# Optimization experiments

Hardware: AMD Instinct MI355X
Metric: run time of the kernel (lower is better)

Reference implementation:

```python
import jax, jax.numpy as jnp
import numpy as np

TEMP = 0.07


def setup_inputs() -> dict:
    key = jax.random.key(0)
    k1, k2 = jax.random.split(key)
    B, m, d = 256, 128, 768
    v_final = jax.random.normal(k1, (B, d), dtype=jnp.float32)
    T_fused = jax.random.normal(k2, (B, m, d), dtype=jnp.float32)
    return {"v_final": v_final, "T_fused": T_fused}


def reference(v_final, T_fused):
    B = v_final.shape[0]
    # [B, B, m] token-level similarities, scaled by temperature
    sim = jnp.einsum('id,jmd->ijm', v_final, T_fused) / TEMP
    # max over text tokens (ColBERT max-sim) -> [B, B]
    sim_max = sim.max(axis=-1)
    targets = jnp.arange(B)
    # symmetric cross-entropy with diagonal targets
    logp_i2t = jax.nn.log_softmax(sim_max, axis=-1)
    logp_t2i = jax.nn.log_softmax(sim_max.T, axis=-1)
    loss_i2t = -jnp.mean(logp_i2t[targets, targets])
    loss_t2i = -jnp.mean(logp_t2i[targets, targets])
    return (loss_i2t + loss_t2i) / 2
```

## Files before the change

kernel.cpp:

```cpp
#include <hip/hip_runtime.h>
#include <hip/hip_bf16.h>

constexpr int BATCH = 256;
constexpr int MTOK  = 128;
constexpr int DDIM  = 768;
constexpr int NV    = BATCH * DDIM;
constexpr float INV_TEMP = 1.0f / 0.07f;

typedef __bf16 bf16;
typedef __bf16 bf16x8 __attribute__((ext_vector_type(8)));
typedef float  f32x4  __attribute__((ext_vector_type(4)));

__global__ __launch_bounds__(256) void pack_v_kernel(
        const float* __restrict__ V, bf16x8* __restrict__ Vq) {
    int c = blockIdx.x * 256 + threadIdx.x;
    int lane = c & 63, fs = c >> 6;
    int ks = fs % 24, g = fs / 24;
    int l15 = lane & 15, quad = lane >> 4;
    const float* src = V + (size_t)(g * 16 + l15) * DDIM + ks * 32 + quad * 8;
    float4 f0 = *(const float4*)(src);
    float4 f1 = *(const float4*)(src + 4);
    bf16x8 o;
    o[0] = (bf16)f0.x; o[1] = (bf16)f0.y; o[2] = (bf16)f0.z; o[3] = (bf16)f0.w;
    o[4] = (bf16)f1.x; o[5] = (bf16)f1.y; o[6] = (bf16)f1.z; o[7] = (bf16)f1.w;
    Vq[c] = o;
}

__global__ __launch_bounds__(256, 2) void gemm_max_kernel(
        const bf16*  __restrict__ Vq,
        const float* __restrict__ T,
        float* __restrict__ Sp) {
    __shared__ char  ldsB[2 * 8192];
    __shared__ float smax[256];

    const int jt   = blockIdx.x >> 1;
    const int nh   = blockIdx.x & 1;
    const int tid  = threadIdx.x;
    const int w    = tid >> 6;
    const int lane = tid & 63;
    const int quad = lane >> 4;
    const int l15  = lane & 15;

    const bf16* aBase[4];
#pragma unroll
    for (int t = 0; t < 4; ++t)
        aBase[t] = Vq + ((size_t)(w * 4 + t) * 24) * 512 + lane * 8;

    const float* gB[2];
    int bwoff[2];
#pragma unroll
    for (int q = 0; q < 2; ++q) {
        int c = q * 256 + tid;
        int row = c >> 3, kp = c & 7;
        gB[q] = T + (size_t)(jt * MTOK + nh * 64 + row) * DDIM + kp * 8;
        bwoff[q] = (kp >> 2) * 4096 + row * 64 + ((kp & 3) << 4);
    }

    int boff[2][4];
#pragma unroll
    for (int h = 0; h < 2; ++h)
#pragma unroll
        for (int tc = 0; tc < 4; ++tc)
            boff[h][tc] = h * 4096 + (tc * 16 + l15) * 64 + quad * 16;

    f32x4 acc[4][4] = {};

    auto cvt_store = [&](float4 a, float4 b, int q, int bufo) {
        bf16x8 o;
        o[0] = (bf16)a.x; o[1] = (bf16)a.y; o[2] = (bf16)a.z; o[3] = (bf16)a.w;
        o[4] = (bf16)b.x; o[5] = (bf16)b.y; o[6] = (bf16)b.z; o[7] = (bf16)b.w;
        *(bf16x8*)(ldsB + bufo + bwoff[q]) = o;
    };

    float4 breg[2][2];
#pragma unroll
    for (int q = 0; q < 2; ++q) {
        float4 r0 = *(const float4*)(gB[q]);
        float4 r1 = *(const float4*)(gB[q] + 4);
        cvt_store(r0, r1, q, 0);
        breg[q][0] = *(const float4*)(gB[q] + 64);
        breg[q][1] = *(const float4*)(gB[q] + 64 + 4);
    }
    bf16x8 apre[2][4];
#pragma unroll
    for (int h = 0; h < 2; ++h)
#pragma unroll
        for (int t = 0; t < 4; ++t)
            apre[h][t] = *(const bf16x8*)(aBase[t] + (size_t)h * 512);
    __syncthreads();

    for (int kk = 0; kk < 12; ++kk) {
        const int buf  = (kk & 1) * 8192;
        const int nbuf = buf ^ 8192;
        if (kk < 11) {
#pragma unroll
            for (int q = 0; q < 2; ++q)
                cvt_store(breg[q][0], breg[q][1], q, nbuf);
        }
        if (kk < 10) {
#pragma unroll
            for (int q = 0; q < 2; ++q) {
                const float* p = gB[q] + (kk + 2) * 64;
                breg[q][0] = *(const float4*)(p);
                breg[q][1] = *(const float4*)(p + 4);
            }
        }
#pragma unroll
        for (int h = 0; h < 2; ++h) {
            const int hs = kk * 2 + h;
            bf16x8 af[4], bb[4];
#pragma unroll
            for (int t = 0; t < 4; ++t) af[t] = apre[h][t];
            if (hs + 2 < 24) {
#pragma unroll
                for (int t = 0; t < 4; ++t)
                    apre[h][t] = *(const bf16x8*)(aBase[t] + (size_t)(hs + 2) * 512);
            }
#pragma unroll
            for (int tc = 0; tc < 4; ++tc)
                bb[tc] = *(const bf16x8*)(ldsB + buf + boff[h][tc]);
#pragma unroll
            for (int tr = 0; tr < 4; ++tr)
#pragma unroll
                for (int tc = 0; tc < 4; ++tc)
                    acc[tr][tc] = __builtin_amdgcn_mfma_f32_16x16x32_bf16(
                        af[tr], bb[tc], acc[tr][tc], 0, 0, 0);
        }
        __syncthreads();
    }

#pragma unroll
    for (int tr = 0; tr < 4; ++tr) {
#pragma unroll
        for (int r = 0; r < 4; ++r) {
            float v = fmaxf(fmaxf(acc[tr][0][r], acc[tr][1][r]),
                            fmaxf(acc[tr][2][r], acc[tr][3][r]));
            v = fmaxf(v, __shfl_xor(v, 1, 64));
            v = fmaxf(v, __shfl_xor(v, 2, 64));
            v = fmaxf(v, __shfl_xor(v, 4, 64));
            v = fmaxf(v, __shfl_xor(v, 8, 64));
            if (l15 == 0)
                smax[w * 64 + tr * 16 + quad * 4 + r] = v;
        }
    }
    __syncthreads();
    Sp[((size_t)nh * BATCH + jt) * BATCH + tid] = smax[tid] * INV_TEMP;
}

__global__ __launch_bounds__(64) void ce1_kernel(
        const float* __restrict__ Sp, float* __restrict__ partial) {
    const int t = blockIdx.x;
    const int l = threadIdx.x;
    const float* Sp0 = Sp;
    const float* Sp1 = Sp + BATCH * BATCH;

    float vr[4], vc[4];
#pragma unroll
    for (int p = 0; p < 4; ++p) {
        int j = p * 64 + l;
        vr[p] = fmaxf(Sp0[j * BATCH + t], Sp1[j * BATCH + t]);
        int i = p * 64 + l;
        vc[p] = fmaxf(Sp0[t * BATCH + i], Sp1[t * BATCH + i]);
    }
    float mr = fmaxf(fmaxf(vr[0], vr[1]), fmaxf(vr[2], vr[3]));
    float mc = fmaxf(fmaxf(vc[0], vc[1]), fmaxf(vc[2], vc[3]));
    for (int o = 32; o > 0; o >>= 1) {
        mr = fmaxf(mr, __shfl_xor(mr, o, 64));
        mc = fmaxf(mc, __shfl_xor(mc, o, 64));
    }
    float sr = 0.f, sc = 0.f;
#pragma unroll
    for (int p = 0; p < 4; ++p) {
        sr += expf(vr[p] - mr);
        sc += expf(vc[p] - mc);
    }
    for (int o = 32; o > 0; o >>= 1) {
        sr += __shfl_xor(sr, o, 64);
        sc += __shfl_xor(sc, o, 64);
    }
    if (l == 0) {
        float diag = fmaxf(Sp0[t * BATCH + t], Sp1[t * BATCH + t]);
        partial[t] = 0.5f * ((mr + logf(sr)) + (mc + logf(sc))) - diag;
    }
}

__global__ __launch_bounds__(256) void ce2_kernel(
        const float* __restrict__ partial, float* __restrict__ out) {
    const int i = threadIdx.x;
    float term = partial[i];
    for (int o = 32; o > 0; o >>= 1) term += __shfl_down(term, o, 64);
    __shared__ float ps[4];
    if ((i & 63) == 0) ps[i >> 6] = term;
    __syncthreads();
    if (i == 0) out[0] = (ps[0] + ps[1] + ps[2] + ps[3]) / (float)BATCH;
}

extern "C" void kernel_launch(void* const* d_in, const int* in_sizes, int n_in,
                              void* d_out, int out_size, void* d_ws, size_t ws_size,
                              hipStream_t stream) {
    const float* v = (const float*)d_in[0];
    const float* T = (const float*)d_in[1];

    bf16*  Vq = (bf16*)d_ws;
    float* Sp = (float*)((char*)d_ws + (size_t)NV * sizeof(bf16));
    float* partial = Sp + 2 * BATCH * BATCH;

    pack_v_kernel<<<96, 256, 0, stream>>>(v, (bf16x8*)Vq);
    gemm_max_kernel<<<512, 256, 0, stream>>>(Vq, T, Sp);
    ce1_kernel<<<256, 64, 0, stream>>>(Sp, partial);
    ce2_kernel<<<1, 256, 0, stream>>>(partial, (float*)d_out);
}
```

Baseline: 163.5 us.

## Deepen GEMM LDS pipeline to four slabs and fuse CE reduction via atomics

The GEMM kernel's B-tile staging moves from a double buffer to a four-slab LDS ring. Two k-slabs are prefetched into registers and converted per iteration, which halves the number of __syncthreads and puts more global loads in flight. Separately, the final loss reduction kernel is removed: the out scalar is zeroed in the pack kernel and each CE block atomically adds its scaled term, saving one launch. The extra LDS and registers may cut occupancy, and the atomic float sum makes the result order-dependent.

```diff
diff --git a/kernel.cpp b/kernel.cpp
--- a/kernel.cpp
+++ b/kernel.cpp
@@ -12,7 +12,9 @@
 typedef float  f32x4  __attribute__((ext_vector_type(4)));
 
 __global__ __launch_bounds__(256) void pack_v_kernel(
-        const float* __restrict__ V, bf16x8* __restrict__ Vq) {
+        const float* __restrict__ V, bf16x8* __restrict__ Vq,
+        float* __restrict__ out) {
+    if (blockIdx.x == 0 && threadIdx.x == 0) out[0] = 0.f;
     int c = blockIdx.x * 256 + threadIdx.x;
     int lane = c & 63, fs = c >> 6;
     int ks = fs % 24, g = fs / 24;
@@ -30,7 +32,7 @@
         const bf16*  __restrict__ Vq,
         const float* __restrict__ T,
         float* __restrict__ Sp) {
-    __shared__ char  ldsB[2 * 8192];
+    __shared__ char  ldsB[4 * 8192];
     __shared__ float smax[256];
 
     const int jt   = blockIdx.x >> 1;
@@ -56,31 +58,33 @@
         bwoff[q] = (kp >> 2) * 4096 + row * 64 + ((kp & 3) << 4);
     }
 
-    int boff[2][4];
-#pragma unroll
-    for (int h = 0; h < 2; ++h)
-#pragma unroll
-        for (int tc = 0; tc < 4; ++tc)
-            boff[h][tc] = h * 4096 + (tc * 16 + l15) * 64 + quad * 16;
+    int boff[4];
+#pragma unroll
+    for (int tc = 0; tc < 4; ++tc)
+        boff[tc] = (tc * 16 + l15) * 64 + quad * 16;
 
     f32x4 acc[4][4] = {};
 
-    auto cvt_store = [&](float4 a, float4 b, int q, int bufo) {
+    auto cvt_store = [&](const float4* r, int q, int bufo) {
         bf16x8 o;
-        o[0] = (bf16)a.x; o[1] = (bf16)a.y; o[2] = (bf16)a.z; o[3] = (bf16)a.w;
-        o[4] = (bf16)b.x; o[5] = (bf16)b.y; o[6] = (bf16)b.z; o[7] = (bf16)b.w;
+        o[0] = (bf16)r[0].x; o[1] = (bf16)r[0].y; o[2] = (bf16)r[0].z; o[3] = (bf16)r[0].w;
+        o[4] = (bf16)r[1].x; o[5] = (bf16)r[1].y; o[6] = (bf16)r[1].z; o[7] = (bf16)r[1].w;
         *(bf16x8*)(ldsB + bufo + bwoff[q]) = o;
     };
 
-    float4 breg[2][2];
-#pragma unroll
-    for (int q = 0; q < 2; ++q) {
-        float4 r0 = *(const float4*)(gB[q]);
-        float4 r1 = *(const float4*)(gB[q] + 4);
-        cvt_store(r0, r1, q, 0);
-        breg[q][0] = *(const float4*)(gB[q] + 64);
-        breg[q][1] = *(const float4*)(gB[q] + 64 + 4);
-    }
+    float4 breg[2][2][2];
+
+#pragma unroll
+    for (int sp = 0; sp < 2; ++sp)
+#pragma unroll
+        for (int q = 0; q < 2; ++q) {
+            float4 r[2];
+            r[0] = *(const float4*)(gB[q] + sp * 64);
+            r[1] = *(const float4*)(gB[q] + sp * 64 + 4);
+            cvt_store(r, q, sp * 8192);
+            breg[sp][q][0] = *(const float4*)(gB[q] + (sp + 2) * 64);
+            breg[sp][q][1] = *(const float4*)(gB[q] + (sp + 2) * 64 + 4);
+        }
     bf16x8 apre[2][4];
 #pragma unroll
     for (int h = 0; h < 2; ++h)
@@ -89,36 +93,40 @@
             apre[h][t] = *(const bf16x8*)(aBase[t] + (size_t)h * 512);
     __syncthreads();
 
-    for (int kk = 0; kk < 12; ++kk) {
-        const int buf  = (kk & 1) * 8192;
-        const int nbuf = buf ^ 8192;
-        if (kk < 11) {
-#pragma unroll
-            for (int q = 0; q < 2; ++q)
-                cvt_store(breg[q][0], breg[q][1], q, nbuf);
-        }
-        if (kk < 10) {
-#pragma unroll
-            for (int q = 0; q < 2; ++q) {
-                const float* p = gB[q] + (kk + 2) * 64;
-                breg[q][0] = *(const float4*)(p);
-                breg[q][1] = *(const float4*)(p + 4);
+    for (int p = 0; p < 6; ++p) {
+        if (p < 5) {
+#pragma unroll
+            for (int sp = 0; sp < 2; ++sp)
+#pragma unroll
+                for (int q = 0; q < 2; ++q)
+                    cvt_store(breg[sp][q], q, ((2 * p + 2 + sp) & 3) * 8192);
+        }
+        if (p < 4) {
+#pragma unroll
+            for (int sp = 0; sp < 2; ++sp)
+#pragma unroll
+                for (int q = 0; q < 2; ++q) {
+                    const float* ptr = gB[q] + (2 * p + 4 + sp) * 64;
+                    breg[sp][q][0] = *(const float4*)(ptr);
+                    breg[sp][q][1] = *(const float4*)(ptr + 4);
+                }
+        }
+#pragma unroll
+        for (int hh = 0; hh < 4; ++hh) {
+            const int hs   = p * 4 + hh;
+            const int slab = hs >> 1;
+            const int bbase = (slab & 3) * 8192 + (hs & 1) * 4096;
+            bf16x8 af[4], bb[4];
+#pragma unroll
+            for (int t = 0; t < 4; ++t) af[t] = apre[hh & 1][t];
+            if (hs + 2 < 24) {
+#pragma unroll
+                for (int t = 0; t < 4; ++t)
+                    apre[hh & 1][t] = *(const bf16x8*)(aBase[t] + (size_t)(hs + 2) * 512);
             }
-        }
-#pragma unroll
-        for (int h = 0; h < 2; ++h) {
-            const int hs = kk * 2 + h;
-            bf16x8 af[4], bb[4];
-#pragma unroll
-            for (int t = 0; t < 4; ++t) af[t] = apre[h][t];
-            if (hs + 2 < 24) {
-#pragma unroll
-                for (int t = 0; t < 4; ++t)
-                    apre[h][t] = *(const bf16x8*)(aBase[t] + (size_t)(hs + 2) * 512);
-            }
 #pragma unroll
             for (int tc = 0; tc < 4; ++tc)
-                bb[tc] = *(const bf16x8*)(ldsB + buf + boff[h][tc]);
+                bb[tc] = *(const bf16x8*)(ldsB + bbase + boff[tc]);
 #pragma unroll
             for (int tr = 0; tr < 4; ++tr)
 #pragma unroll
@@ -126,7 +134,7 @@
                     acc[tr][tc] = __builtin_amdgcn_mfma_f32_16x16x32_bf16(
                         af[tr], bb[tc], acc[tr][tc], 0, 0, 0);
         }
-        __syncthreads();
+        if (p < 5) __syncthreads();
     }
 
 #pragma unroll
@@ -147,8 +155,8 @@
     Sp[((size_t)nh * BATCH + jt) * BATCH + tid] = smax[tid] * INV_TEMP;
 }
 
-__global__ __launch_bounds__(64) void ce1_kernel(
-        const float* __restrict__ Sp, float* __restrict__ partial) {
+__global__ __launch_bounds__(64) void ce_kernel(
+        const float* __restrict__ Sp, float* __restrict__ out) {
     const int t = blockIdx.x;
     const int l = threadIdx.x;
     const float* Sp0 = Sp;
@@ -180,19 +188,9 @@
     }
     if (l == 0) {
         float diag = fmaxf(Sp0[t * BATCH + t], Sp1[t * BATCH + t]);
-        partial[t] = 0.5f * ((mr + logf(sr)) + (mc + logf(sc))) - diag;
-    }
-}
-
-__global__ __launch_bounds__(256) void ce2_kernel(
-        const float* __restrict__ partial, float* __restrict__ out) {
-    const int i = threadIdx.x;
-    float term = partial[i];
-    for (int o = 32; o > 0; o >>= 1) term += __shfl_down(term, o, 64);
-    __shared__ float ps[4];
-    if ((i & 63) == 0) ps[i >> 6] = term;
-    __syncthreads();
-    if (i == 0) out[0] = (ps[0] + ps[1] + ps[2] + ps[3]) / (float)BATCH;
+        float term = 0.5f * ((mr + logf(sr)) + (mc + logf(sc))) - diag;
+        atomicAdd(out, term * (1.0f / (float)BATCH));
+    }
 }
 
 extern "C" void kernel_launch(void* const* d_in, const int* in_sizes, int n_in,
@@ -203,10 +201,8 @@
 
     bf16*  Vq = (bf16*)d_ws;
     float* Sp = (float*)((char*)d_ws + (size_t)NV * sizeof(bf16));
-    float* partial = Sp + 2 * BATCH * BATCH;
-
-    pack_v_kernel<<<96, 256, 0, stream>>>(v, (bf16x8*)Vq);
+
+    pack_v_kernel<<<96, 256, 0, stream>>>(v, (bf16x8*)Vq, (float*)d_out);
     gemm_max_kernel<<<512, 256, 0, stream>>>(Vq, T, Sp);
-    ce1_kernel<<<256, 64, 0, stream>>>(Sp, partial);
-    ce2_kernel<<<1, 256, 0, stream>>>(partial, (float*)d_out);
-}
+    ce_kernel<<<256, 64, 0, stream>>>(Sp, (float*)d_out);
+}
```

Result: no change. 163.9 us (+0.3%).
